# Kernel tuning notes

Hardware: AMD Instinct MI355X
Metric: run time of the kernel (lower is better)

Reference implementation:

```python
import jax, jax.numpy as jnp
import numpy as np

B, NQ, NK = 4, 2048, 2048
D_MODEL, D_K, D_V, H = 1024, 1024, 1024, 16


def setup_inputs() -> dict:
    key = jax.random.key(0)
    ks = jax.random.split(key, 8)
    return {
        "queries": jax.random.normal(ks[0], (B, NQ, D_MODEL), dtype=jnp.float32),
        "keys": jax.random.normal(ks[1], (B, NK, D_MODEL), dtype=jnp.float32),
        "values": jax.random.normal(ks[2], (B, NK, D_MODEL), dtype=jnp.float32),
        # nn.Linear weights init.normal_(std=0.001); stored here in (in, out) layout
        "Wq": jax.random.normal(ks[3], (D_MODEL, D_K), dtype=jnp.float32) * 0.001,
        "Wk": jax.random.normal(ks[4], (D_MODEL, D_K), dtype=jnp.float32) * 0.001,
        "Wv": jax.random.normal(ks[5], (D_MODEL, D_V), dtype=jnp.float32) * 0.001,
        "Wo": jax.random.normal(ks[6], (D_V, D_MODEL), dtype=jnp.float32) * 0.001,
        "bo": jnp.zeros((D_MODEL,), dtype=jnp.float32),
    }


def reference(queries, keys, values, Wq, Wk, Wv, Wo, bo):
    b_s, nq, _ = queries.shape
    nk = keys.shape[1]
    hd_k = D_K // H  # per-head key dim
    hd_v = D_V // H  # per-head value dim
    # projections -> [b, h, n, hd]
    q = (queries @ Wq).reshape(b_s, nq, H, hd_k).transpose(0, 2, 1, 3)
    k = (keys @ Wk).reshape(b_s, nk, H, hd_k).transpose(0, 2, 1, 3)
    v = (values @ Wv).reshape(b_s, nk, H, hd_v).transpose(0, 2, 1, 3)
    # NOTE: original scales by sqrt(d_k) (full d_k), not per-head dim
    att = jnp.einsum("bhqd,bhkd->bhqk", q, k) / np.float32(np.sqrt(D_K))
    att = jax.nn.softmax(att, axis=-1)
    # dropout = identity (eval mode)
    out = jnp.einsum("bhqk,bhkd->bhqd", att, v)
    out = out.transpose(0, 2, 1, 3).reshape(b_s, nq, D_V)
    return out @ Wo + bo
```

## Files before the change

### kernel.cpp

```cpp
#include <hip/hip_runtime.h>


#define DM    1024
#define NSEQ  2048
#define HEADS 16
#define HD    64

typedef float floatx4 __attribute__((ext_vector_type(4)));
typedef short s16x4   __attribute__((ext_vector_type(4)));
typedef short s16x8   __attribute__((ext_vector_type(8)));
typedef unsigned int u32x4 __attribute__((ext_vector_type(4)));

static __device__ __forceinline__ floatx4 mfma_bf16(s16x8 a, s16x8 b, floatx4 c) {
  return __builtin_amdgcn_mfma_f32_16x16x32_bf16(a, b, c, 0, 0, 0);
}

static __device__ __forceinline__ void gload_lds16(const void* g, void* l) {
  __builtin_amdgcn_global_load_lds(
      (const __attribute__((address_space(1))) unsigned*)g,
      (__attribute__((address_space(3))) unsigned*)l, 16, 0, 0);
}

static __device__ __forceinline__ unsigned lds_addr(const void* p) {
  return (unsigned)(unsigned long long)p;
}

static __device__ __forceinline__ s16x8 ds_read_b128a(unsigned byteaddr) {
  s16x8 r;
  asm volatile("ds_read_b128 %0, %1" : "=v"(r) : "v"(byteaddr));
  return r;
}

#define WAIT_LGKM0() \
  { asm volatile("s_waitcnt lgkmcnt(0)" ::: "memory"); __builtin_amdgcn_sched_barrier(0); }

static __device__ __forceinline__ short f2bf(float f) {
  unsigned u = __builtin_bit_cast(unsigned, f);
  u += 0x7FFFu + ((u >> 16) & 1u);
  return (short)(u >> 16);
}

static __device__ __forceinline__ unsigned cvtpk_bf16(float lo, float hi) {
  unsigned r;
  asm("v_cvt_pk_bf16_f32 %0, %1, %2" : "=v"(r) : "v"(lo), "v"(hi));
  return r;
}

static __device__ __forceinline__ unsigned pack2_bf16(float a, float b) {
  unsigned ua = __builtin_bit_cast(unsigned, a) + 0x8000u;
  unsigned ub = __builtin_bit_cast(unsigned, b) + 0x8000u;
#if __has_builtin(__builtin_amdgcn_perm)
  return __builtin_amdgcn_perm(ub, ua, 0x07060302u);
#else
  return (ub & 0xffff0000u) | (ua >> 16);
#endif
}

__global__ __launch_bounds__(256) void transpose_cast_w(
    const float* __restrict__ W0, const float* __restrict__ W1,
    const float* __restrict__ W2, const float* __restrict__ W3,
    short* __restrict__ T0, short* __restrict__ T1,
    short* __restrict__ T2, short* __restrict__ T3) {
  __shared__ float tile[32][33];
  const float* W = blockIdx.z == 0 ? W0 : blockIdx.z == 1 ? W1 : blockIdx.z == 2 ? W2 : W3;
  short*       T = blockIdx.z == 0 ? T0 : blockIdx.z == 1 ? T1 : blockIdx.z == 2 ? T2 : T3;
  const int bx = blockIdx.x * 32;
  const int by = blockIdx.y * 32;
  const int tx = threadIdx.x, ty = threadIdx.y;
  for (int i = 0; i < 4; i++)
    tile[ty + i * 8][tx] = W[(long)(by + ty + i * 8) * DM + bx + tx];
  __syncthreads();
  for (int i = 0; i < 4; i++)
    T[(long)(bx + ty + i * 8) * DM + by + tx] = f2bf(tile[tx][ty + i * 8]);
}

__global__ __launch_bounds__(512, 2) void proj_kernel(
    const float* __restrict__ Aq, const float* __restrict__ Ak, const float* __restrict__ Av,
    const short* __restrict__ BtQ, const short* __restrict__ BtK, const short* __restrict__ BtV,
    short* __restrict__ Qh, short* __restrict__ Kh, short* __restrict__ Vt) {
  __shared__ short lds[2 * 32768];
  const int z = blockIdx.z;
  const float* A  = z == 0 ? Aq  : z == 1 ? Ak  : Av;
  const short* Bt = z == 0 ? BtQ : z == 1 ? BtK : BtV;
  const int t = threadIdx.x;
  const int w = t >> 6, l = t & 63, quad = l >> 4, lm = l & 15;
  const int wm = w >> 2, wn = w & 3;
  const int row0 = blockIdx.x * 128, col0 = blockIdx.y * 256;

  floatx4 acc[4][4];
  for (int mi = 0; mi < 4; mi++)
    for (int ni = 0; ni < 4; ni++) acc[mi][ni] = (floatx4){0.f, 0.f, 0.f, 0.f};

  auto stage = [&](int k0, int buf) __attribute__((always_inline)) {
    short* base = lds + buf * 32768;
#pragma unroll
    for (int i = 0; i < 4; i++) {
      int ga = w * 4 + i, g16 = ga >> 2, kk = (ga >> 1) & 1, h = ga & 1;
      const float* src =
          A + (long)(row0 + g16 * 16 + lm) * DM + k0 + kk * 32 + quad * 8 + h * 4;
      gload_lds16(src, base + ga * 512);
    }
#pragma unroll
    for (int i = 0; i < 4; i++) {
      int gb = w * 4 + i, g16c = gb >> 1, kk = gb & 1;
      const short* src =
          Bt + (long)(col0 + g16c * 16 + lm) * DM + k0 + kk * 32 + quad * 8;
      gload_lds16(src, base + 16384 + gb * 512);
    }
  };

  const unsigned lds0 = lds_addr(lds);
  auto process = [&](int buf) __attribute__((always_inline)) {
    const unsigned lbase = lds0 + buf * 65536;
#pragma unroll
    for (int kk = 0; kk < 2; kk++) {
      floatx4 alo[4], ahi[4];
      s16x8 bfr[4];
#pragma unroll
      for (int mi = 0; mi < 4; mi++) {
        unsigned ga0 = ((wm * 4 + mi) * 4 + kk * 2) * 1024;
        alo[mi] = __builtin_bit_cast(floatx4, ds_read_b128a(lbase + ga0 + l * 16));
        ahi[mi] = __builtin_bit_cast(floatx4, ds_read_b128a(lbase + ga0 + 1024 + l * 16));
      }
#pragma unroll
      for (int ni = 0; ni < 4; ni++) {
        unsigned gb0 = 32768u + ((wn * 4 + ni) * 2 + kk) * 1024;
        bfr[ni] = ds_read_b128a(lbase + gb0 + l * 16);
      }
      WAIT_LGKM0();
      s16x8 af[4];
#pragma unroll
      for (int mi = 0; mi < 4; mi++) {
        u32x4 p = {cvtpk_bf16(alo[mi][0], alo[mi][1]), cvtpk_bf16(alo[mi][2], alo[mi][3]),
                   cvtpk_bf16(ahi[mi][0], ahi[mi][1]), cvtpk_bf16(ahi[mi][2], ahi[mi][3])};
        af[mi] = __builtin_bit_cast(s16x8, p);
      }
      __builtin_amdgcn_s_setprio(1);
#pragma unroll
      for (int mi = 0; mi < 4; mi++)
#pragma unroll
        for (int ni = 0; ni < 4; ni++)
          acc[mi][ni] = mfma_bf16(af[mi], bfr[ni], acc[mi][ni]);
      __builtin_amdgcn_s_setprio(0);
    }
  };

  stage(0, 0);
  __syncthreads();
  int cur = 0;
  for (int tt = 0; tt < 16; ++tt) {
    if (tt + 1 < 16) stage((tt + 1) * 64, cur ^ 1);
    process(cur);
    __syncthreads();
    cur ^= 1;
  }

  const int rowbase = row0 + wm * 64;
  const int colbase = col0 + wn * 64;
  const int b = rowbase >> 11;
  const int h = colbase >> 6;
  const int rloc = rowbase & 2047;
  if (z < 2) {
    short* Out = z == 0 ? Qh : Kh;
    const float osc = z == 0 ? 0.0450842200277801f : 1.0f;
    long base = ((long)(b * HEADS + h)) * NSEQ * HD;
    for (int mi = 0; mi < 4; mi++)
      for (int r = 0; r < 4; r++) {
        int q = rloc + mi * 16 + quad * 4 + r;
        long rowoff = base + (long)q * HD + lm;
        for (int ni = 0; ni < 4; ni++)
          Out[rowoff + ni * 16] = f2bf(acc[mi][ni][r] * osc);
      }
  } else {
    long base = ((long)(b * HEADS + h)) * HD * NSEQ;
    for (int mi = 0; mi < 4; mi++)
      for (int r = 0; r < 4; r++) {
        int kcol = rloc + (mi >> 1) * 32 + quad * 8 + (mi & 1) * 4 + r;
        for (int ni = 0; ni < 4; ni++)
          Vt[base + (long)(ni * 16 + lm) * NSEQ + kcol] = f2bf(acc[mi][ni][r]);
      }
  }
}

__global__ __launch_bounds__(256, 2) void attn_kernel(
    const short* __restrict__ Qh, const short* __restrict__ Kh,
    const short* __restrict__ Vt, short* __restrict__ Obf) {
  __shared__ short lds[2 * 16384];
  const int t = threadIdx.x;
  const int w = t >> 6, l = t & 63, quad = l >> 4, lm = l & 15;
  const int bh = blockIdx.x;
  const int qtile = blockIdx.y * 128 + w * 32;
  const short* Qp = Qh + (long)bh * NSEQ * HD;
  const short* Kp = Kh + (long)bh * NSEQ * HD;
  const short* Vp = Vt + (long)bh * HD * NSEQ;

  s16x8 aq[2][2];
#pragma unroll
  for (int qi = 0; qi < 2; qi++)
#pragma unroll
    for (int c = 0; c < 2; c++)
      aq[qi][c] = *(const s16x8*)(Qp + (long)(qtile + qi * 16 + lm) * HD + c * 32 + quad * 8);

  floatx4 acc[2][4];
  float lsum[2] = {0.f, 0.f};
#pragma unroll
  for (int qi = 0; qi < 2; qi++)
#pragma unroll
    for (int n = 0; n < 4; n++) acc[qi][n] = (floatx4){0.f, 0.f, 0.f, 0.f};

  auto stage = [&](int kt, int buf) __attribute__((always_inline)) {
    short* base = lds + buf * 16384;
#pragma unroll
    for (int i = 0; i < 8; i++) {
      int g = w * 8 + i;
      const short* src;
      if (w < 2) {
        int s = g >> 2, j = (g >> 1) & 1, c = g & 1;
        src = Kp + (long)(kt + s * 32 + j * 16 + lm) * HD + c * 32 + quad * 8;
      } else {
        int gg = g & 15;
        int s = gg >> 2, n = gg & 3;
        src = Vp + (long)(n * 16 + lm) * NSEQ + kt + s * 32 + quad * 8;
      }
      gload_lds16(src, base + g * 512);
    }
  };

  auto process = [&](const short* Lb, int s) __attribute__((always_inline)) {
    s16x8 bk[2][2];
#pragma unroll
    for (int j = 0; j < 2; j++)
#pragma unroll
      for (int c = 0; c < 2; c++)
        bk[j][c] = *(const s16x8*)(Lb + ((s * 4 + j * 2 + c) * 64 + l) * 8);
    s16x8 vraw[4];
#pragma unroll
    for (int n = 0; n < 4; n++)
      vraw[n] = *(const s16x8*)(Lb + ((16 + s * 4 + n) * 64 + l) * 8);
#pragma unroll
    for (int qi = 0; qi < 2; qi++) {
      floatx4 sT[2];
      sT[0] = (floatx4){0.f, 0.f, 0.f, 0.f};
      sT[1] = (floatx4){0.f, 0.f, 0.f, 0.f};
      __builtin_amdgcn_s_setprio(1);
#pragma unroll
      for (int c = 0; c < 2; c++) {
        sT[0] = mfma_bf16(bk[0][c], aq[qi][c], sT[0]);
        sT[1] = mfma_bf16(bk[1][c], aq[qi][c], sT[1]);
      }
      __builtin_amdgcn_s_setprio(0);
      float p0 = __builtin_amdgcn_exp2f(sT[0][0]);
      float p1 = __builtin_amdgcn_exp2f(sT[0][1]);
      float p2 = __builtin_amdgcn_exp2f(sT[0][2]);
      float p3 = __builtin_amdgcn_exp2f(sT[0][3]);
      float p4 = __builtin_amdgcn_exp2f(sT[1][0]);
      float p5 = __builtin_amdgcn_exp2f(sT[1][1]);
      float p6 = __builtin_amdgcn_exp2f(sT[1][2]);
      float p7 = __builtin_amdgcn_exp2f(sT[1][3]);
      lsum[qi] += ((p0 + p1) + (p2 + p3)) + ((p4 + p5) + (p6 + p7));
      u32x4 pw = {pack2_bf16(p0, p1), pack2_bf16(p2, p3),
                  pack2_bf16(p4, p5), pack2_bf16(p6, p7)};
      s16x8 pcat = __builtin_bit_cast(s16x8, pw);
      __builtin_amdgcn_s_setprio(1);
#pragma unroll
      for (int n = 0; n < 4; n++)
        acc[qi][n] = mfma_bf16(vraw[n], pcat, acc[qi][n]);
      __builtin_amdgcn_s_setprio(0);
    }
  };

  stage(0, 0);
  __syncthreads();
  int cur = 0;
  for (int kt = 0; kt < NSEQ; kt += 128) {
    if (kt + 128 < NSEQ) stage(kt + 128, cur ^ 1);
    const short* Lb = lds + cur * 16384;
    process(Lb, 0);
    process(Lb, 1);
    process(Lb, 2);
    process(Lb, 3);
    __syncthreads();
    cur ^= 1;
  }

  const int b = bh >> 4, h = bh & 15;
  short* Ow = lds + w * 1152;
  const int erow = l >> 2, ecg = l & 3;
#pragma unroll
  for (int qi = 0; qi < 2; qi++) {
    float ls = lsum[qi];
    ls += __shfl_xor(ls, 16);
    ls += __shfl_xor(ls, 32);
    float rl = 1.0f / ls;
#pragma unroll
    for (int n = 0; n < 4; n++)
#pragma unroll
      for (int r = 0; r < 4; r++)
        Ow[lm * 72 + n * 16 + quad * 4 + r] = f2bf(acc[qi][n][r] * rl);
    s16x8 o0 = *(const s16x8*)(Ow + erow * 72 + ecg * 16);
    s16x8 o1 = *(const s16x8*)(Ow + erow * 72 + ecg * 16 + 8);
    long gaddr = ((long)(b * NSEQ + qtile + qi * 16 + erow)) * DM + h * HD + ecg * 16;
    *(s16x8*)(Obf + gaddr) = o0;
    *(s16x8*)(Obf + gaddr + 8) = o1;
  }
}

__global__ __launch_bounds__(256, 2) void out_kernel(
    const short* __restrict__ Ab, const short* __restrict__ Bt,
    const float* __restrict__ bias, float* __restrict__ Out) {
  __shared__ short lds[2 * 16384];
  const int t = threadIdx.x;
  const int w = t >> 6, l = t & 63, quad = l >> 4, lm = l & 15;
  const int wm = w >> 1, wn = w & 1;
  const int row0 = blockIdx.x * 128, col0 = blockIdx.y * 128;

  floatx4 acc[4][4];
  for (int mi = 0; mi < 4; mi++)
    for (int ni = 0; ni < 4; ni++) acc[mi][ni] = (floatx4){0.f, 0.f, 0.f, 0.f};

  auto stage = [&](int k0, int buf) __attribute__((always_inline)) {
    short* base = lds + buf * 16384;
#pragma unroll
    for (int i = 0; i < 8; i++) {
      int g = w * 8 + i;
      const short* src;
      short* dst;
      if (g < 16) {
        int g16 = g >> 1, kk = g & 1;
        src = Ab + (long)(row0 + g16 * 16 + lm) * DM + k0 + kk * 32 + quad * 8;
        dst = base + g * 512;
      } else {
        int gb = g - 16, g16 = gb >> 1, kk = gb & 1;
        src = Bt + (long)(col0 + g16 * 16 + lm) * DM + k0 + kk * 32 + quad * 8;
        dst = base + 8192 + gb * 512;
      }
      gload_lds16(src, dst);
    }
  };
  const unsigned lds0 = lds_addr(lds);
  auto process = [&](int buf) __attribute__((always_inline)) {
    const unsigned lbase = lds0 + buf * 32768;
#pragma unroll
    for (int kk = 0; kk < 2; kk++) {
      s16x8 af[4], bfr[4];
#pragma unroll
      for (int mi = 0; mi < 4; mi++)
        af[mi] = ds_read_b128a(lbase + ((wm * 4 + mi) * 2 + kk) * 1024 + l * 16);
#pragma unroll
      for (int ni = 0; ni < 4; ni++)
        bfr[ni] = ds_read_b128a(lbase + 16384 + ((wn * 4 + ni) * 2 + kk) * 1024 + l * 16);
      WAIT_LGKM0();
      __builtin_amdgcn_s_setprio(1);
#pragma unroll
      for (int mi = 0; mi < 4; mi++)
#pragma unroll
        for (int ni = 0; ni < 4; ni++)
          acc[mi][ni] = mfma_bf16(af[mi], bfr[ni], acc[mi][ni]);
      __builtin_amdgcn_s_setprio(0);
    }
  };

  stage(0, 0);
  __syncthreads();
  int cur = 0;
  for (int tt = 0; tt < 16; ++tt) {
    if (tt + 1 < 16) stage((tt + 1) * 64, cur ^ 1);
    process(cur);
    __syncthreads();
    cur ^= 1;
  }

  const int rowbase = row0 + wm * 64;
  const int colbase = col0 + wn * 64;
  for (int mi = 0; mi < 4; mi++)
    for (int r = 0; r < 4; r++) {
      int gr = rowbase + mi * 16 + quad * 4 + r;
      for (int ni = 0; ni < 4; ni++) {
        int gc = colbase + ni * 16 + lm;
        Out[(long)gr * DM + gc] = acc[mi][ni][r] + bias[gc];
      }
    }
}

extern "C" void kernel_launch(void* const* d_in, const int* in_sizes, int n_in,
                              void* d_out, int out_size, void* d_ws, size_t ws_size,
                              hipStream_t stream) {
  (void)in_sizes; (void)n_in; (void)out_size; (void)ws_size;
  const float* queries = (const float*)d_in[0];
  const float* keys    = (const float*)d_in[1];
  const float* values  = (const float*)d_in[2];
  const float* Wq = (const float*)d_in[3];
  const float* Wk = (const float*)d_in[4];
  const float* Wv = (const float*)d_in[5];
  const float* Wo = (const float*)d_in[6];
  const float* bo = (const float*)d_in[7];
  float* out = (float*)d_out;

  char* ws = (char*)d_ws;
  const size_t MB = 1024 * 1024;
  short* WqT = (short*)(ws + 0 * MB);
  short* WkT = (short*)(ws + 2 * MB);
  short* WvT = (short*)(ws + 4 * MB);
  short* WoT = (short*)(ws + 6 * MB);
  short* Qh  = (short*)(ws + 8 * MB);
  short* Kh  = (short*)(ws + 24 * MB);
  short* Vt  = (short*)(ws + 40 * MB);
  short* Obf = (short*)(ws + 56 * MB);

  transpose_cast_w<<<dim3(32, 32, 4), dim3(32, 8), 0, stream>>>(
      Wq, Wk, Wv, Wo, WqT, WkT, WvT, WoT);
  proj_kernel<<<dim3(64, 4, 3), 512, 0, stream>>>(
      queries, keys, values, WqT, WkT, WvT, Qh, Kh, Vt);
  attn_kernel<<<dim3(64, 16), 256, 0, stream>>>(Qh, Kh, Vt, Obf);
  out_kernel<<<dim3(64, 8), 256, 0, stream>>>(Obf, WoT, bo, out);
}
```

Before: 374.7 us.

## Pre-tile weights and K/V into MFMA-fragment order; register-stage A with bf16 LDS

Weights are now written in a pre-grouped tile layout so every B-operand stage becomes contiguous 16-byte global-to-LDS copies. K and V projections are written interleaved per 128-key tile, so the attention kernel stages each tile with one contiguous copy. The fp32 A operand in the projection kernel is loaded through registers, converted to bf16 before being stored to LDS, and stored with an XOR swizzle; this halves A's LDS footprint and removes conversions from the inner loop. The cost is more complex scatter stores in the epilogues and register pressure from prefetched A data.

```diff
diff --git a/kernel.cpp b/kernel.cpp
--- a/kernel.cpp
+++ b/kernel.cpp
@@ -56,85 +56,105 @@
 #endif
 }
 
-__global__ __launch_bounds__(256) void transpose_cast_w(
+__global__ __launch_bounds__(256) void make_wgroups(
     const float* __restrict__ W0, const float* __restrict__ W1,
     const float* __restrict__ W2, const float* __restrict__ W3,
-    short* __restrict__ T0, short* __restrict__ T1,
-    short* __restrict__ T2, short* __restrict__ T3) {
-  __shared__ float tile[32][33];
-  const float* W = blockIdx.z == 0 ? W0 : blockIdx.z == 1 ? W1 : blockIdx.z == 2 ? W2 : W3;
-  short*       T = blockIdx.z == 0 ? T0 : blockIdx.z == 1 ? T1 : blockIdx.z == 2 ? T2 : T3;
-  const int bx = blockIdx.x * 32;
-  const int by = blockIdx.y * 32;
-  const int tx = threadIdx.x, ty = threadIdx.y;
-  for (int i = 0; i < 4; i++)
-    tile[ty + i * 8][tx] = W[(long)(by + ty + i * 8) * DM + bx + tx];
+    short* __restrict__ G0, short* __restrict__ G1,
+    short* __restrict__ G2, short* __restrict__ G3) {
+  __shared__ float tile[64][68];
+  const int m = blockIdx.z;
+  const float* W = m == 0 ? W0 : m == 1 ? W1 : m == 2 ? W2 : W3;
+  short*       G = m == 0 ? G0 : m == 1 ? G1 : m == 2 ? G2 : G3;
+  const int nt = blockIdx.x, kt = blockIdx.y;
+  const int n0 = nt * 64, k0 = kt * 64;
+  const int t = threadIdx.x;
+  for (int j = 0; j < 4; j++) {
+    int idx = j * 256 + t, r = idx >> 4, cq = idx & 15;
+    *(floatx4*)&tile[r][cq * 4] = *(const floatx4*)(W + (long)(k0 + r) * DM + n0 + cq * 4);
+  }
   __syncthreads();
-  for (int i = 0; i < 4; i++)
-    T[(long)(bx + ty + i * 8) * DM + by + tx] = f2bf(tile[tx][ty + i * 8]);
+  for (int j = 0; j < 2; j++) {
+    int ci = j * 256 + t;
+    int lm = ci & 15, quad = (ci >> 4) & 3, kk = (ci >> 6) & 1, gl = ci >> 7;
+    s16x8 v;
+#pragma unroll
+    for (int e = 0; e < 8; e++) v[e] = f2bf(tile[kk * 32 + quad * 8 + e][gl * 16 + lm]);
+    long addr;
+    if (m < 3) {
+      int ct = nt >> 2, g16 = (nt & 3) * 4 + gl;
+      addr = ((long)(ct * 16 + kt)) * 16384 + (g16 * 2 + kk) * 512 + (quad * 16 + lm) * 8;
+    } else {
+      int ct = nt >> 1, g16 = (nt & 1) * 4 + gl;
+      addr = ((long)(ct * 16 + kt)) * 8192 + (g16 * 2 + kk) * 512 + (quad * 16 + lm) * 8;
+    }
+    *(s16x8*)(G + addr) = v;
+  }
 }
 
 __global__ __launch_bounds__(512, 2) void proj_kernel(
     const float* __restrict__ Aq, const float* __restrict__ Ak, const float* __restrict__ Av,
-    const short* __restrict__ BtQ, const short* __restrict__ BtK, const short* __restrict__ BtV,
-    short* __restrict__ Qh, short* __restrict__ Kh, short* __restrict__ Vt) {
-  __shared__ short lds[2 * 32768];
+    const short* __restrict__ BgQ, const short* __restrict__ BgK, const short* __restrict__ BgV,
+    short* __restrict__ Qh, short* __restrict__ KVg) {
+  __shared__ short lds[2 * 24576];
   const int z = blockIdx.z;
   const float* A  = z == 0 ? Aq  : z == 1 ? Ak  : Av;
-  const short* Bt = z == 0 ? BtQ : z == 1 ? BtK : BtV;
+  const short* Bg = z == 0 ? BgQ : z == 1 ? BgK : BgV;
   const int t = threadIdx.x;
   const int w = t >> 6, l = t & 63, quad = l >> 4, lm = l & 15;
   const int wm = w >> 2, wn = w & 3;
-  const int row0 = blockIdx.x * 128, col0 = blockIdx.y * 256;
+  const int row0 = blockIdx.x * 128;
+  const int ct = blockIdx.y;
+  const int col0 = ct * 256;
 
   floatx4 acc[4][4];
   for (int mi = 0; mi < 4; mi++)
     for (int ni = 0; ni < 4; ni++) acc[mi][ni] = (floatx4){0.f, 0.f, 0.f, 0.f};
 
-  auto stage = [&](int k0, int buf) __attribute__((always_inline)) {
-    short* base = lds + buf * 32768;
+  floatx4 ar[2][2];
+  auto loadA = [&](int ks) __attribute__((always_inline)) {
+#pragma unroll
+    for (int j = 0; j < 2; j++) {
+      int tt = j * 512 + t, r = tt >> 3, c8 = (tt & 7) * 8;
+      const float* p = A + (long)(row0 + r) * DM + ks * 64 + c8;
+      ar[j][0] = *(const floatx4*)p;
+      ar[j][1] = *(const floatx4*)(p + 4);
+    }
+  };
+  auto writeA = [&](int buf) __attribute__((always_inline)) {
+#pragma unroll
+    for (int j = 0; j < 2; j++) {
+      int tt = j * 512 + t, r = tt >> 3;
+      int kk = (tt & 7) >> 2, q4 = tt & 3, lm2 = r & 15, g16 = r >> 4;
+      u32x4 pk = {cvtpk_bf16(ar[j][0][0], ar[j][0][1]), cvtpk_bf16(ar[j][0][2], ar[j][0][3]),
+                  cvtpk_bf16(ar[j][1][0], ar[j][1][1]), cvtpk_bf16(ar[j][1][2], ar[j][1][3])};
+      int l3 = q4 * 16 + (lm2 ^ (q4 * 2));
+      *(s16x8*)(lds + buf * 24576 + (g16 * 2 + kk) * 512 + l3 * 8) =
+          __builtin_bit_cast(s16x8, pk);
+    }
+  };
+  auto stageB = [&](int ks, int buf) __attribute__((always_inline)) {
 #pragma unroll
     for (int i = 0; i < 4; i++) {
-      int ga = w * 4 + i, g16 = ga >> 2, kk = (ga >> 1) & 1, h = ga & 1;
-      const float* src =
-          A + (long)(row0 + g16 * 16 + lm) * DM + k0 + kk * 32 + quad * 8 + h * 4;
-      gload_lds16(src, base + ga * 512);
-    }
-#pragma unroll
-    for (int i = 0; i < 4; i++) {
-      int gb = w * 4 + i, g16c = gb >> 1, kk = gb & 1;
-      const short* src =
-          Bt + (long)(col0 + g16c * 16 + lm) * DM + k0 + kk * 32 + quad * 8;
-      gload_lds16(src, base + 16384 + gb * 512);
+      int gb = w * 4 + i;
+      const short* src = Bg + ((long)(ct * 16 + ks)) * 16384 + gb * 512 + l * 8;
+      gload_lds16(src, lds + buf * 24576 + 8192 + gb * 512);
     }
   };
 
   const unsigned lds0 = lds_addr(lds);
   auto process = [&](int buf) __attribute__((always_inline)) {
-    const unsigned lbase = lds0 + buf * 65536;
+    const unsigned lbase = lds0 + buf * 49152;
+    const unsigned aswz = (quad * 16 + (lm ^ (quad * 2))) * 16;
 #pragma unroll
     for (int kk = 0; kk < 2; kk++) {
-      floatx4 alo[4], ahi[4];
-      s16x8 bfr[4];
-#pragma unroll
-      for (int mi = 0; mi < 4; mi++) {
-        unsigned ga0 = ((wm * 4 + mi) * 4 + kk * 2) * 1024;
-        alo[mi] = __builtin_bit_cast(floatx4, ds_read_b128a(lbase + ga0 + l * 16));
-        ahi[mi] = __builtin_bit_cast(floatx4, ds_read_b128a(lbase + ga0 + 1024 + l * 16));
-      }
-#pragma unroll
-      for (int ni = 0; ni < 4; ni++) {
-        unsigned gb0 = 32768u + ((wn * 4 + ni) * 2 + kk) * 1024;
-        bfr[ni] = ds_read_b128a(lbase + gb0 + l * 16);
-      }
+      s16x8 af[4], bfr[4];
+#pragma unroll
+      for (int mi = 0; mi < 4; mi++)
+        af[mi] = ds_read_b128a(lbase + ((wm * 4 + mi) * 2 + kk) * 1024 + aswz);
+#pragma unroll
+      for (int ni = 0; ni < 4; ni++)
+        bfr[ni] = ds_read_b128a(lbase + 16384 + ((wn * 4 + ni) * 2 + kk) * 1024 + l * 16);
       WAIT_LGKM0();
-      s16x8 af[4];
-#pragma unroll
-      for (int mi = 0; mi < 4; mi++) {
-        u32x4 p = {cvtpk_bf16(alo[mi][0], alo[mi][1]), cvtpk_bf16(alo[mi][2], alo[mi][3]),
-                   cvtpk_bf16(ahi[mi][0], ahi[mi][1]), cvtpk_bf16(ahi[mi][2], ahi[mi][3])};
-        af[mi] = __builtin_bit_cast(s16x8, p);
-      }
       __builtin_amdgcn_s_setprio(1);
 #pragma unroll
       for (int mi = 0; mi < 4; mi++)
@@ -145,12 +165,16 @@
     }
   };
 
-  stage(0, 0);
+  loadA(0);
+  stageB(0, 0);
+  writeA(0);
   __syncthreads();
   int cur = 0;
-  for (int tt = 0; tt < 16; ++tt) {
-    if (tt + 1 < 16) stage((tt + 1) * 64, cur ^ 1);
+  for (int ks = 0; ks < 16; ++ks) {
+    if (ks + 1 < 16) { loadA(ks + 1); stageB(ks + 1, cur ^ 1); }
+    __builtin_amdgcn_sched_barrier(0);
     process(cur);
+    if (ks + 1 < 16) writeA(cur ^ 1);
     __syncthreads();
     cur ^= 1;
   }
@@ -160,39 +184,54 @@
   const int b = rowbase >> 11;
   const int h = colbase >> 6;
   const int rloc = rowbase & 2047;
-  if (z < 2) {
-    short* Out = z == 0 ? Qh : Kh;
-    const float osc = z == 0 ? 0.0450842200277801f : 1.0f;
+  if (z == 0) {
+    const float osc = 0.0450842200277801f;
     long base = ((long)(b * HEADS + h)) * NSEQ * HD;
     for (int mi = 0; mi < 4; mi++)
       for (int r = 0; r < 4; r++) {
         int q = rloc + mi * 16 + quad * 4 + r;
         long rowoff = base + (long)q * HD + lm;
         for (int ni = 0; ni < 4; ni++)
-          Out[rowoff + ni * 16] = f2bf(acc[mi][ni][r] * osc);
+          Qh[rowoff + ni * 16] = f2bf(acc[mi][ni][r] * osc);
+      }
+  } else if (z == 1) {
+    long bhb = ((long)(b * HEADS + h)) * 262144;
+    for (int mi = 0; mi < 4; mi++)
+      for (int r = 0; r < 4; r++) {
+        int q = rloc + mi * 16 + quad * 4 + r;
+        int tile = q >> 7, s = (q >> 5) & 3, jj = (q >> 4) & 1, lmk = q & 15;
+        for (int ni = 0; ni < 4; ni++) {
+          int c = ni >> 1, quadk = (ni * 2 + (lm >> 3)) & 3, ek = lm & 7;
+          long addr = bhb + (long)tile * 16384 + (s * 4 + jj * 2 + c) * 512 +
+                      (quadk * 16 + lmk) * 8 + ek;
+          KVg[addr] = f2bf(acc[mi][ni][r]);
+        }
       }
   } else {
-    long base = ((long)(b * HEADS + h)) * HD * NSEQ;
+    long bhb = ((long)(b * HEADS + h)) * 262144;
     for (int mi = 0; mi < 4; mi++)
       for (int r = 0; r < 4; r++) {
-        int kcol = rloc + (mi >> 1) * 32 + quad * 8 + (mi & 1) * 4 + r;
-        for (int ni = 0; ni < 4; ni++)
-          Vt[base + (long)(ni * 16 + lm) * NSEQ + kcol] = f2bf(acc[mi][ni][r]);
+        int kc = rloc + (mi >> 1) * 32 + quad * 8 + (mi & 1) * 4 + r;
+        int tile = kc >> 7, s = (kc >> 5) & 3, ev = (mi & 1) * 4 + r;
+        for (int ni = 0; ni < 4; ni++) {
+          long addr = bhb + (long)tile * 16384 + (16 + s * 4 + ni) * 512 +
+                      (quad * 16 + lm) * 8 + ev;
+          KVg[addr] = f2bf(acc[mi][ni][r]);
+        }
       }
   }
 }
 
 __global__ __launch_bounds__(256, 2) void attn_kernel(
-    const short* __restrict__ Qh, const short* __restrict__ Kh,
-    const short* __restrict__ Vt, short* __restrict__ Obf) {
+    const short* __restrict__ Qh, const short* __restrict__ KVg,
+    short* __restrict__ Obf) {
   __shared__ short lds[2 * 16384];
   const int t = threadIdx.x;
   const int w = t >> 6, l = t & 63, quad = l >> 4, lm = l & 15;
   const int bh = blockIdx.x;
   const int qtile = blockIdx.y * 128 + w * 32;
-  const short* Qp = Qh + (long)bh * NSEQ * HD;
-  const short* Kp = Kh + (long)bh * NSEQ * HD;
-  const short* Vp = Vt + (long)bh * HD * NSEQ;
+  const short* Qp  = Qh  + (long)bh * NSEQ * HD;
+  const short* KVp = KVg + (long)bh * 262144;
 
   s16x8 aq[2][2];
 #pragma unroll
@@ -210,19 +249,11 @@
 
   auto stage = [&](int kt, int buf) __attribute__((always_inline)) {
     short* base = lds + buf * 16384;
+    const short* tsrc = KVp + (long)(kt >> 7) * 16384;
 #pragma unroll
     for (int i = 0; i < 8; i++) {
       int g = w * 8 + i;
-      const short* src;
-      if (w < 2) {
-        int s = g >> 2, j = (g >> 1) & 1, c = g & 1;
-        src = Kp + (long)(kt + s * 32 + j * 16 + lm) * HD + c * 32 + quad * 8;
-      } else {
-        int gg = g & 15;
-        int s = gg >> 2, n = gg & 3;
-        src = Vp + (long)(n * 16 + lm) * NSEQ + kt + s * 32 + quad * 8;
-      }
-      gload_lds16(src, base + g * 512);
+      gload_lds16(tsrc + g * 512 + l * 8, base + g * 512);
     }
   };
 
@@ -306,46 +337,55 @@
 }
 
 __global__ __launch_bounds__(256, 2) void out_kernel(
-    const short* __restrict__ Ab, const short* __restrict__ Bt,
+    const short* __restrict__ Ab, const short* __restrict__ WoG,
     const float* __restrict__ bias, float* __restrict__ Out) {
   __shared__ short lds[2 * 16384];
   const int t = threadIdx.x;
   const int w = t >> 6, l = t & 63, quad = l >> 4, lm = l & 15;
   const int wm = w >> 1, wn = w & 1;
-  const int row0 = blockIdx.x * 128, col0 = blockIdx.y * 128;
+  const int row0 = blockIdx.x * 128;
+  const int ct = blockIdx.y;
+  const int col0 = ct * 128;
 
   floatx4 acc[4][4];
   for (int mi = 0; mi < 4; mi++)
     for (int ni = 0; ni < 4; ni++) acc[mi][ni] = (floatx4){0.f, 0.f, 0.f, 0.f};
 
-  auto stage = [&](int k0, int buf) __attribute__((always_inline)) {
-    short* base = lds + buf * 16384;
-#pragma unroll
-    for (int i = 0; i < 8; i++) {
-      int g = w * 8 + i;
-      const short* src;
-      short* dst;
-      if (g < 16) {
-        int g16 = g >> 1, kk = g & 1;
-        src = Ab + (long)(row0 + g16 * 16 + lm) * DM + k0 + kk * 32 + quad * 8;
-        dst = base + g * 512;
-      } else {
-        int gb = g - 16, g16 = gb >> 1, kk = gb & 1;
-        src = Bt + (long)(col0 + g16 * 16 + lm) * DM + k0 + kk * 32 + quad * 8;
-        dst = base + 8192 + gb * 512;
-      }
-      gload_lds16(src, dst);
+  s16x8 ar[4];
+  auto loadA = [&](int ks) __attribute__((always_inline)) {
+#pragma unroll
+    for (int j = 0; j < 4; j++) {
+      int tt = j * 256 + t, r = tt >> 3, c = tt & 7;
+      ar[j] = *(const s16x8*)(Ab + (long)(row0 + r) * DM + ks * 64 + c * 8);
+    }
+  };
+  auto writeA = [&](int buf) __attribute__((always_inline)) {
+#pragma unroll
+    for (int j = 0; j < 4; j++) {
+      int tt = j * 256 + t, r = tt >> 3, c = tt & 7;
+      int kk = c >> 2, q4 = c & 3, lm2 = r & 15, g16 = r >> 4;
+      int l3 = q4 * 16 + (lm2 ^ (q4 * 2));
+      *(s16x8*)(lds + buf * 16384 + (g16 * 2 + kk) * 512 + l3 * 8) = ar[j];
+    }
+  };
+  auto stageB = [&](int ks, int buf) __attribute__((always_inline)) {
+#pragma unroll
+    for (int i = 0; i < 4; i++) {
+      int gb = w * 4 + i;
+      const short* src = WoG + ((long)(ct * 16 + ks)) * 8192 + gb * 512 + l * 8;
+      gload_lds16(src, lds + buf * 16384 + 8192 + gb * 512);
     }
   };
   const unsigned lds0 = lds_addr(lds);
   auto process = [&](int buf) __attribute__((always_inline)) {
     const unsigned lbase = lds0 + buf * 32768;
+    const unsigned aswz = (quad * 16 + (lm ^ (quad * 2))) * 16;
 #pragma unroll
     for (int kk = 0; kk < 2; kk++) {
       s16x8 af[4], bfr[4];
 #pragma unroll
       for (int mi = 0; mi < 4; mi++)
-        af[mi] = ds_read_b128a(lbase + ((wm * 4 + mi) * 2 + kk) * 1024 + l * 16);
+        af[mi] = ds_read_b128a(lbase + ((wm * 4 + mi) * 2 + kk) * 1024 + aswz);
 #pragma unroll
       for (int ni = 0; ni < 4; ni++)
         bfr[ni] = ds_read_b128a(lbase + 16384 + ((wn * 4 + ni) * 2 + kk) * 1024 + l * 16);
@@ -360,12 +400,16 @@
     }
   };
 
-  stage(0, 0);
+  loadA(0);
+  stageB(0, 0);
+  writeA(0);
   __syncthreads();
   int cur = 0;
-  for (int tt = 0; tt < 16; ++tt) {
-    if (tt + 1 < 16) stage((tt + 1) * 64, cur ^ 1);
+  for (int ks = 0; ks < 16; ++ks) {
+    if (ks + 1 < 16) { loadA(ks + 1); stageB(ks + 1, cur ^ 1); }
+    __builtin_amdgcn_sched_barrier(0);
     process(cur);
+    if (ks + 1 < 16) writeA(cur ^ 1);
     __syncthreads();
     cur ^= 1;
   }
@@ -398,19 +442,18 @@
 
   char* ws = (char*)d_ws;
   const size_t MB = 1024 * 1024;
-  short* WqT = (short*)(ws + 0 * MB);
-  short* WkT = (short*)(ws + 2 * MB);
-  short* WvT = (short*)(ws + 4 * MB);
-  short* WoT = (short*)(ws + 6 * MB);
+  short* WqG = (short*)(ws + 0 * MB);
+  short* WkG = (short*)(ws + 2 * MB);
+  short* WvG = (short*)(ws + 4 * MB);
+  short* WoG = (short*)(ws + 6 * MB);
   short* Qh  = (short*)(ws + 8 * MB);
-  short* Kh  = (short*)(ws + 24 * MB);
-  short* Vt  = (short*)(ws + 40 * MB);
+  short* KVg = (short*)(ws + 24 * MB);
   short* Obf = (short*)(ws + 56 * MB);
 
-  transpose_cast_w<<<dim3(32, 32, 4), dim3(32, 8), 0, stream>>>(
-      Wq, Wk, Wv, Wo, WqT, WkT, WvT, WoT);
+  make_wgroups<<<dim3(16, 16, 4), 256, 0, stream>>>(
+      Wq, Wk, Wv, Wo, WqG, WkG, WvG, WoG);
   proj_kernel<<<dim3(64, 4, 3), 512, 0, stream>>>(
-      queries, keys, values, WqT, WkT, WvT, Qh, Kh, Vt);
-  attn_kernel<<<dim3(64, 16), 256, 0, stream>>>(Qh, Kh, Vt, Obf);
-  out_kernel<<<dim3(64, 8), 256, 0, stream>>>(Obf, WoT, bo, out);
-}
+      queries, keys, values, WqG, WkG, WvG, Qh, KVg);
+  attn_kernel<<<dim3(64, 16), 256, 0, stream>>>(Qh, KVg, Obf);
+  out_kernel<<<dim3(64, 8), 256, 0, stream>>>(Obf, WoG, bo, out);
+}
```

New measurement: 318.5 us. -15.0%, faster.
